# Kernel tuning notes

Hardware: AMD Instinct MI355X
Metric: run time of the kernel (lower is better)

Reference implementation:

```python
import jax, jax.numpy as jnp
import numpy as np


def setup_inputs() -> dict:
    key = jax.random.key(0)
    k1, k2 = jax.random.split(key)
    N, C, H, W = 8, 512, 64, 64
    K = 64
    x = jax.random.normal(k1, (N, C, H, W), dtype=jnp.float32)
    y = jax.random.normal(k2, (N, K, H, W), dtype=jnp.float32)
    scale = jnp.zeros((1,), dtype=jnp.float32)
    return {"x": x, "y": y, "scale": scale}


def reference(x, y, scale):
    N, C, H, W = x.shape
    K = y.shape[1]
    HW = H * W
    xq = x.reshape(N, C, HW)            # (N, C, HW) queries (channel-wise)
    yk = y.reshape(N, K, HW)            # (N, K, HW) keys/values
    # energy: (N, C, K)
    energy = jnp.einsum('ncs,nks->nck', xq, yk)
    # inverted max-subtraction: softmax(max_k(E) - E) over last dim
    energy_new = jnp.max(energy, axis=-1, keepdims=True) - energy
    attention = jax.nn.softmax(energy_new, axis=-1)  # (N, C, K)
    out = jnp.einsum('nck,nks->ncs', attention, yk)   # (N, C, HW)
    out = out.reshape(N, C, H, W)
    return x + scale * out
```

## Files before the change

### kernel.cpp

```cpp
#include <hip/hip_runtime.h>

#define N_ 8
#define C_ 512
#define K_ 64
#define HW_ 4096
#define SCHUNK 128
#define NCH 32

typedef __attribute__((ext_vector_type(8))) short short8;
typedef __attribute__((ext_vector_type(4))) float floatx4;

__device__ __forceinline__ short8 cvt8(const float* __restrict__ p){
  float4 u = *(const float4*)p;
  float4 w = *(const float4*)(p + 4);
  union { unsigned u32[4]; short8 s; } r;
  asm("v_cvt_pk_bf16_f32 %0, %1, %2" : "=v"(r.u32[0]) : "v"(u.x), "v"(u.y));
  asm("v_cvt_pk_bf16_f32 %0, %1, %2" : "=v"(r.u32[1]) : "v"(u.z), "v"(u.w));
  asm("v_cvt_pk_bf16_f32 %0, %1, %2" : "=v"(r.u32[2]) : "v"(w.x), "v"(w.y));
  asm("v_cvt_pk_bf16_f32 %0, %1, %2" : "=v"(r.u32[3]) : "v"(w.z), "v"(w.w));
  return r.s;
}

__device__ __forceinline__ void gload16(const void* g, void* l){
  __builtin_amdgcn_global_load_lds(
      (const __attribute__((address_space(1))) void*)g,
      (__attribute__((address_space(3))) void*)l, 16, 0, 0);
}

__global__ __launch_bounds__(256) void k_prep(const float* __restrict__ y,
                                              unsigned short* __restrict__ ybf,
                                              unsigned short* __restrict__ ytr){
  __shared__ unsigned short tile[64][72];
  int n  = blockIdx.x >> 6;
  int s0 = (blockIdx.x & 63) << 6;
  int tid = threadIdx.x;
  int k  = tid >> 2;
  int sc = (tid & 3) << 4;
  const float* yp = y + ((size_t)n * K_ + k) * HW_ + s0 + sc;
  union { unsigned short u16[16]; short8 s8[2]; uint4 q[2]; } u;
  u.s8[0] = cvt8(yp);
  u.s8[1] = cvt8(yp + 8);
  unsigned short* rp = ybf + ((size_t)n * K_ + k) * HW_ + s0 + sc;
  *(uint4*)rp       = u.q[0];
  *(uint4*)(rp + 8) = u.q[1];
#pragma unroll
  for (int j = 0; j < 16; ++j) tile[sc + j][k] = u.u16[j];
  __syncthreads();
  int s  = tid >> 2;
  int kc = (tid & 3) << 4;
  unsigned short* tp = ytr + ((size_t)n * HW_ + s0 + s) * K_ + kc;
  *(uint4*)tp       = *(const uint4*)&tile[s][kc];
  *(uint4*)(tp + 8) = *(const uint4*)&tile[s][kc + 8];
}

__global__ __launch_bounds__(512, 1) void k_fused(const float* __restrict__ x,
                                                  const unsigned short* __restrict__ ybf,
                                                  const unsigned short* __restrict__ ytr,
                                                  const float* __restrict__ scale,
                                                  float* __restrict__ out){
  __shared__ char As[4][8192];
  __shared__ char Bs[4][16384];
  __shared__ float Els[2][16][64];
  __shared__ char attl[2048];
  __shared__ float T[8][16][68];

  const int bid = ((blockIdx.x & 7) << 5) | (blockIdx.x >> 3);
  const int ct = bid & 31, n = bid >> 5;
  const int tid = threadIdx.x;
  const int w = tid >> 6, l = tid & 63;
  const int lo = l & 15, hi = l >> 4;
  const int h = w >> 2, q = w & 3;
  const int c0 = ct << 4;

  float sc = scale[0];
  asm volatile("" :: "v"(sc));

  const int ar = (w << 1) + (l >> 5);
  const char* asrc = (const char*)(x + ((size_t)n * C_ + c0 + ar) * HW_)
                     + ((16 * (l & 31)) ^ ((ar & 7) << 4));
  const int kb0 = ((w << 1) + 0) * 4 + (l >> 4);
  const int kb1 = ((w << 1) + 1) * 4 + (l >> 4);
  const char* bsrc0 = (const char*)(ybf + ((size_t)n * K_ + kb0) * HW_)
                      + ((16 * (l & 15)) ^ ((kb0 & 7) << 4));
  const char* bsrc1 = (const char*)(ybf + ((size_t)n * K_ + kb1) * HW_)
                      + ((16 * (l & 15)) ^ ((kb1 & 7) << 4));

  floatx4 acc = {0.f, 0.f, 0.f, 0.f};
  const int aswz = (lo & 7) << 4;
  const int brow = (q << 4) + lo;

#define STAGE(BUF, CH)                                                          \
  {                                                                             \
    gload16(asrc  + (size_t)(CH) * (SCHUNK * 4), As[BUF] + (w << 10));          \
    gload16(bsrc0 + (size_t)(CH) * (SCHUNK * 2), Bs[BUF] + ((w << 1) << 10));   \
    gload16(bsrc1 + (size_t)(CH) * (SCHUNK * 2), Bs[BUF] + ((((w << 1) | 1)) << 10)); \
  }

  STAGE(0, 0) STAGE(1, 1) STAGE(2, 2)

#pragma unroll
  for (int ch = 0; ch < NCH; ++ch){
    const int cur = ch & 3;
    if (ch + 3 < NCH){
      STAGE((ch + 3) & 3, ch + 3)
      asm volatile("s_waitcnt vmcnt(9)" ::: "memory");
    } else if (ch + 2 < NCH){
      asm volatile("s_waitcnt vmcnt(6)" ::: "memory");
    } else if (ch + 1 < NCH){
      asm volatile("s_waitcnt vmcnt(3)" ::: "memory");
    } else {
      asm volatile("s_waitcnt vmcnt(0)" ::: "memory");
    }
    __builtin_amdgcn_s_barrier();
    __builtin_amdgcn_sched_barrier(0);
#pragma unroll
    for (int ss = 0; ss < 2; ++ss){
      int ao = (h << 8) + (ss << 7) + (hi << 5);
      const char* ab = As[cur] + (lo << 9);
      float4 a0f = *(const float4*)(ab + ((ao     ) ^ aswz));
      float4 a1f = *(const float4*)(ab + ((ao + 16) ^ aswz));
      union { unsigned u32[4]; short8 s; } af;
      asm("v_cvt_pk_bf16_f32 %0, %1, %2" : "=v"(af.u32[0]) : "v"(a0f.x), "v"(a0f.y));
      asm("v_cvt_pk_bf16_f32 %0, %1, %2" : "=v"(af.u32[1]) : "v"(a0f.z), "v"(a0f.w));
      asm("v_cvt_pk_bf16_f32 %0, %1, %2" : "=v"(af.u32[2]) : "v"(a1f.x), "v"(a1f.y));
      asm("v_cvt_pk_bf16_f32 %0, %1, %2" : "=v"(af.u32[3]) : "v"(a1f.z), "v"(a1f.w));
      int bo = (h << 7) + (ss << 6) + (hi << 4);
      short8 b = *(const short8*)(Bs[cur] + brow * 256 + (bo ^ aswz));
      acc = __builtin_amdgcn_mfma_f32_16x16x32_bf16(b, af.s, acc, 0, 0, 0);
    }
    __builtin_amdgcn_sched_barrier(0);
    __builtin_amdgcn_s_barrier();
  }
#undef STAGE

  *(floatx4*)&Els[h][lo][(q << 4) + (hi << 2)] = acc;
  __syncthreads();

  if (tid < 256){
    int c = tid >> 4, j = tid & 15;
    float4 t0 = *(const float4*)&Els[0][c][4 * j];
    float4 t1 = *(const float4*)&Els[1][c][4 * j];
    float e0 = t0.x + t1.x, e1 = t0.y + t1.y, e2 = t0.z + t1.z, e3 = t0.w + t1.w;
    float m = fminf(fminf(e0, e1), fminf(e2, e3));
#pragma unroll
    for (int off = 8; off; off >>= 1) m = fminf(m, __shfl_xor(m, off, 16));
    float p0 = __expf(m - e0), p1 = __expf(m - e1);
    float p2 = __expf(m - e2), p3 = __expf(m - e3);
    float s = p0 + p1 + p2 + p3;
#pragma unroll
    for (int off = 8; off; off >>= 1) s += __shfl_xor(s, off, 16);
    float inv = 1.f / s;
    unsigned d0, d1;
    asm("v_cvt_pk_bf16_f32 %0, %1, %2" : "=v"(d0) : "v"(p0 * inv), "v"(p1 * inv));
    asm("v_cvt_pk_bf16_f32 %0, %1, %2" : "=v"(d1) : "v"(p2 * inv), "v"(p3 * inv));
    uint2 dd; dd.x = d0; dd.y = d1;
    *(uint2*)(attl + c * 128 + ((8 * j) ^ ((c & 7) << 4))) = dd;
  }
  __syncthreads();

  short8 batt0 = *(const short8*)(attl + lo * 128 + ((     hi * 16) ^ ((lo & 7) << 4)));
  short8 batt1 = *(const short8*)(attl + lo * 128 + ((64 + hi * 16) ^ ((lo & 7) << 4)));
  const unsigned short* ybn = ytr + (size_t)n * HW_ * K_;
  const int sW = w << 9;
  float (*Tw)[68] = T[w];
  size_t xb[4];
#pragma unroll
  for (int rg = 0; rg < 4; ++rg)
    xb[rg] = ((size_t)n * C_ + c0 + (rg << 2) + hi) * HW_ + sW + (lo << 2);

  short8 aA[8]; float4 xA[4];
  short8 aB[8]; float4 xB[4];

#define PVLOAD(G, AV, XV)                                                      \
  {                                                                            \
    int sg = sW + (G) * 64;                                                    \
    _Pragma("unroll")                                                          \
    for (int t = 0; t < 4; ++t){                                               \
      const unsigned short* ap = ybn + (size_t)(sg + t * 16 + lo) * K_ + (hi << 3); \
      AV[2 * t]     = *(const short8*)(ap);                                    \
      AV[2 * t + 1] = *(const short8*)(ap + 32);                               \
    }                                                                          \
    _Pragma("unroll")                                                          \
    for (int rg = 0; rg < 4; ++rg)                                             \
      XV[rg] = *(const float4*)(x + xb[rg] + (G) * 64);                        \
  }

#define PVCOMP(G, AV, XV)                                                      \
  {                                                                            \
    _Pragma("unroll")                                                          \
    for (int t = 0; t < 4; ++t){                                               \
      floatx4 a2 = {0.f, 0.f, 0.f, 0.f};                                       \
      a2 = __builtin_amdgcn_mfma_f32_16x16x32_bf16(AV[2 * t],     batt0, a2, 0, 0, 0); \
      a2 = __builtin_amdgcn_mfma_f32_16x16x32_bf16(AV[2 * t + 1], batt1, a2, 0, 0, 0); \
      *(floatx4*)&Tw[lo][t * 16 + (hi << 2)] = a2;    \
    }                                                                          \
    _Pragma("unroll")                                                          \
    for (int rg = 0; rg < 4; ++rg){                                            \
      float4 v  = *(const float4*)&Tw[(rg << 2) + hi][lo << 2];                \
      float4 xv = XV[rg];                                                      \
      float4 o;                                                                \
      o.x = xv.x + sc * v.x; o.y = xv.y + sc * v.y;                            \
      o.z = xv.z + sc * v.z; o.w = xv.w + sc * v.w;                            \
      *(float4*)(out + xb[rg] + (G) * 64) = o;                                 \
    }                                                                          \
  }

  PVLOAD(0, aA, xA)
#pragma unroll
  for (int g = 0; g < 8; g += 2){
    PVLOAD(g + 1, aB, xB)
    PVCOMP(g, aA, xA)
    if (g + 2 < 8) PVLOAD(g + 2, aA, xA)
    PVCOMP(g + 1, aB, xB)
  }
#undef PVLOAD
#undef PVCOMP
}

extern "C" void kernel_launch(void* const* d_in, const int* in_sizes, int n_in,
                              void* d_out, int out_size, void* d_ws, size_t ws_size,
                              hipStream_t stream){
  const float* x     = (const float*)d_in[0];
  const float* y     = (const float*)d_in[1];
  const float* scale = (const float*)d_in[2];
  float* out = (float*)d_out;

  char* ws = (char*)d_ws;
  unsigned short* ybf = (unsigned short*)(ws);
  unsigned short* ytr = (unsigned short*)(ws + (4u<<20));

  k_prep  <<<N_ * (HW_/64), 256, 0, stream>>>(y, ybf, ytr);
  k_fused <<<N_ * 32,       512, 0, stream>>>(x, ybf, ytr, scale, out);
}
```

Baseline: 52.00 us.

## Split spatial reduction across block pairs with global partial-energy exchange

Each (n, channel-tile) is now handled by two blocks, each reducing half of the spatial dimension. The blocks exchange partial energy sums through a global buffer, synchronising with an atomic flag and a spin wait. This doubles the grid so more of the device's compute units get work, and it cuts the LDS pipeline to two stages so more blocks fit. The cost is an inter-block dependency that relies on both partner blocks being co-resident, plus an extra memset and global traffic.

```diff
diff --git a/kernel.cpp b/kernel.cpp
--- a/kernel.cpp
+++ b/kernel.cpp
@@ -5,7 +5,7 @@
 #define K_ 64
 #define HW_ 4096
 #define SCHUNK 128
-#define NCH 32
+#define NCH 16
 
 typedef __attribute__((ext_vector_type(8))) short short8;
 typedef __attribute__((ext_vector_type(4))) float floatx4;
@@ -53,60 +53,58 @@
   *(uint4*)(tp + 8) = *(const uint4*)&tile[s][kc + 8];
 }
 
-__global__ __launch_bounds__(512, 1) void k_fused(const float* __restrict__ x,
+__global__ __launch_bounds__(512, 4) void k_fused(const float* __restrict__ x,
                                                   const unsigned short* __restrict__ ybf,
                                                   const unsigned short* __restrict__ ytr,
                                                   const float* __restrict__ scale,
+                                                  unsigned* __restrict__ flags,
+                                                  float* __restrict__ epart,
                                                   float* __restrict__ out){
-  __shared__ char As[4][8192];
-  __shared__ char Bs[4][16384];
-  __shared__ float Els[2][16][64];
-  __shared__ char attl[2048];
-  __shared__ float T[8][16][68];
-
-  const int bid = ((blockIdx.x & 7) << 5) | (blockIdx.x >> 3);
-  const int ct = bid & 31, n = bid >> 5;
+  __shared__ char smem[49152];
+
+  const int b = blockIdx.x;
+  const int n = b >> 6, ct = (b >> 1) & 31, half = b & 1;
   const int tid = threadIdx.x;
   const int w = tid >> 6, l = tid & 63;
   const int lo = l & 15, hi = l >> 4;
   const int h = w >> 2, q = w & 3;
   const int c0 = ct << 4;
+  const int sb = half << 11;
+  const int pairid = (n << 5) + ct;
 
   float sc = scale[0];
   asm volatile("" :: "v"(sc));
 
   const int ar = (w << 1) + (l >> 5);
-  const char* asrc = (const char*)(x + ((size_t)n * C_ + c0 + ar) * HW_)
+  const char* asrc = (const char*)(x + ((size_t)n * C_ + c0 + ar) * HW_ + sb)
                      + ((16 * (l & 31)) ^ ((ar & 7) << 4));
   const int kb0 = ((w << 1) + 0) * 4 + (l >> 4);
   const int kb1 = ((w << 1) + 1) * 4 + (l >> 4);
-  const char* bsrc0 = (const char*)(ybf + ((size_t)n * K_ + kb0) * HW_)
+  const char* bsrc0 = (const char*)(ybf + ((size_t)n * K_ + kb0) * HW_ + sb)
                       + ((16 * (l & 15)) ^ ((kb0 & 7) << 4));
-  const char* bsrc1 = (const char*)(ybf + ((size_t)n * K_ + kb1) * HW_)
+  const char* bsrc1 = (const char*)(ybf + ((size_t)n * K_ + kb1) * HW_ + sb)
                       + ((16 * (l & 15)) ^ ((kb1 & 7) << 4));
 
   floatx4 acc = {0.f, 0.f, 0.f, 0.f};
   const int aswz = (lo & 7) << 4;
   const int brow = (q << 4) + lo;
 
-#define STAGE(BUF, CH)                                                          \
-  {                                                                             \
-    gload16(asrc  + (size_t)(CH) * (SCHUNK * 4), As[BUF] + (w << 10));          \
-    gload16(bsrc0 + (size_t)(CH) * (SCHUNK * 2), Bs[BUF] + ((w << 1) << 10));   \
-    gload16(bsrc1 + (size_t)(CH) * (SCHUNK * 2), Bs[BUF] + ((((w << 1) | 1)) << 10)); \
-  }
-
-  STAGE(0, 0) STAGE(1, 1) STAGE(2, 2)
+#define AS(BUF) (smem + (BUF) * 24576)
+#define BS(BUF) (smem + (BUF) * 24576 + 8192)
+#define STAGE(BUF, CH)                                                         \
+  {                                                                            \
+    gload16(asrc  + (size_t)(CH) * (SCHUNK * 4), AS(BUF) + (w << 10));         \
+    gload16(bsrc0 + (size_t)(CH) * (SCHUNK * 2), BS(BUF) + ((w << 1) << 10));  \
+    gload16(bsrc1 + (size_t)(CH) * (SCHUNK * 2), BS(BUF) + (((w << 1) | 1) << 10)); \
+  }
+
+  STAGE(0, 0)
 
 #pragma unroll
   for (int ch = 0; ch < NCH; ++ch){
-    const int cur = ch & 3;
-    if (ch + 3 < NCH){
-      STAGE((ch + 3) & 3, ch + 3)
-      asm volatile("s_waitcnt vmcnt(9)" ::: "memory");
-    } else if (ch + 2 < NCH){
-      asm volatile("s_waitcnt vmcnt(6)" ::: "memory");
-    } else if (ch + 1 < NCH){
+    const int cur = ch & 1;
+    if (ch + 1 < NCH){
+      STAGE(cur ^ 1, ch + 1)
       asm volatile("s_waitcnt vmcnt(3)" ::: "memory");
     } else {
       asm volatile("s_waitcnt vmcnt(0)" ::: "memory");
@@ -116,7 +114,7 @@
 #pragma unroll
     for (int ss = 0; ss < 2; ++ss){
       int ao = (h << 8) + (ss << 7) + (hi << 5);
-      const char* ab = As[cur] + (lo << 9);
+      const char* ab = AS(cur) + (lo << 9);
       float4 a0f = *(const float4*)(ab + ((ao     ) ^ aswz));
       float4 a1f = *(const float4*)(ab + ((ao + 16) ^ aswz));
       union { unsigned u32[4]; short8 s; } af;
@@ -125,22 +123,47 @@
       asm("v_cvt_pk_bf16_f32 %0, %1, %2" : "=v"(af.u32[2]) : "v"(a1f.x), "v"(a1f.y));
       asm("v_cvt_pk_bf16_f32 %0, %1, %2" : "=v"(af.u32[3]) : "v"(a1f.z), "v"(a1f.w));
       int bo = (h << 7) + (ss << 6) + (hi << 4);
-      short8 b = *(const short8*)(Bs[cur] + brow * 256 + (bo ^ aswz));
-      acc = __builtin_amdgcn_mfma_f32_16x16x32_bf16(b, af.s, acc, 0, 0, 0);
+      short8 bfr = *(const short8*)(BS(cur) + brow * 256 + (bo ^ aswz));
+      acc = __builtin_amdgcn_mfma_f32_16x16x32_bf16(bfr, af.s, acc, 0, 0, 0);
     }
     __builtin_amdgcn_sched_barrier(0);
     __builtin_amdgcn_s_barrier();
   }
 #undef STAGE
 
+  float (*Els)[16][64] = (float (*)[16][64])smem;
   *(floatx4*)&Els[h][lo][(q << 4) + (hi << 2)] = acc;
   __syncthreads();
 
+  float e0 = 0.f, e1 = 0.f, e2 = 0.f, e3 = 0.f;
   if (tid < 256){
+    float4 t0 = *(const float4*)&Els[0][tid >> 4][(tid & 15) * 4];
+    float4 t1 = *(const float4*)&Els[1][tid >> 4][(tid & 15) * 4];
+    e0 = t0.x + t1.x; e1 = t0.y + t1.y; e2 = t0.z + t1.z; e3 = t0.w + t1.w;
+    float* ep = epart + (((size_t)pairid << 1) + half) * 1024 + (tid << 2);
+    __hip_atomic_store(ep + 0, e0, __ATOMIC_RELAXED, __HIP_MEMORY_SCOPE_AGENT);
+    __hip_atomic_store(ep + 1, e1, __ATOMIC_RELAXED, __HIP_MEMORY_SCOPE_AGENT);
+    __hip_atomic_store(ep + 2, e2, __ATOMIC_RELAXED, __HIP_MEMORY_SCOPE_AGENT);
+    __hip_atomic_store(ep + 3, e3, __ATOMIC_RELAXED, __HIP_MEMORY_SCOPE_AGENT);
+  }
+  __threadfence();
+  __syncthreads();
+  if (tid == 0){
+    atomicAdd(&flags[pairid], 1u);
+    while (atomicAdd(&flags[pairid], 0u) < 2u)
+      __builtin_amdgcn_s_sleep(1);
+  }
+  __syncthreads();
+  __threadfence();
+
+  char* attl = smem + 8192;
+  if (tid < 256){
+    const float* ep = epart + (((size_t)pairid << 1) + (half ^ 1)) * 1024 + (tid << 2);
+    e0 += __hip_atomic_load(ep + 0, __ATOMIC_RELAXED, __HIP_MEMORY_SCOPE_AGENT);
+    e1 += __hip_atomic_load(ep + 1, __ATOMIC_RELAXED, __HIP_MEMORY_SCOPE_AGENT);
+    e2 += __hip_atomic_load(ep + 2, __ATOMIC_RELAXED, __HIP_MEMORY_SCOPE_AGENT);
+    e3 += __hip_atomic_load(ep + 3, __ATOMIC_RELAXED, __HIP_MEMORY_SCOPE_AGENT);
     int c = tid >> 4, j = tid & 15;
-    float4 t0 = *(const float4*)&Els[0][c][4 * j];
-    float4 t1 = *(const float4*)&Els[1][c][4 * j];
-    float e0 = t0.x + t1.x, e1 = t0.y + t1.y, e2 = t0.z + t1.z, e3 = t0.w + t1.w;
     float m = fminf(fminf(e0, e1), fminf(e2, e3));
 #pragma unroll
     for (int off = 8; off; off >>= 1) m = fminf(m, __shfl_xor(m, off, 16));
@@ -161,19 +184,19 @@
   short8 batt0 = *(const short8*)(attl + lo * 128 + ((     hi * 16) ^ ((lo & 7) << 4)));
   short8 batt1 = *(const short8*)(attl + lo * 128 + ((64 + hi * 16) ^ ((lo & 7) << 4)));
   const unsigned short* ybn = ytr + (size_t)n * HW_ * K_;
-  const int sW = w << 9;
-  float (*Tw)[68] = T[w];
+  const int sP = sb + (w << 8);
+  float (*Tw)[68] = (float (*)[68])(smem + 16384 + w * 4352);
   size_t xb[4];
 #pragma unroll
   for (int rg = 0; rg < 4; ++rg)
-    xb[rg] = ((size_t)n * C_ + c0 + (rg << 2) + hi) * HW_ + sW + (lo << 2);
+    xb[rg] = ((size_t)n * C_ + c0 + (rg << 2) + hi) * HW_ + sP + (lo << 2);
 
   short8 aA[8]; float4 xA[4];
   short8 aB[8]; float4 xB[4];
 
 #define PVLOAD(G, AV, XV)                                                      \
   {                                                                            \
-    int sg = sW + (G) * 64;                                                    \
+    int sg = sP + (G) * 64;                                                    \
     _Pragma("unroll")                                                          \
     for (int t = 0; t < 4; ++t){                                               \
       const unsigned short* ap = ybn + (size_t)(sg + t * 16 + lo) * K_ + (hi << 3); \
@@ -206,15 +229,17 @@
   }
 
   PVLOAD(0, aA, xA)
-#pragma unroll
-  for (int g = 0; g < 8; g += 2){
-    PVLOAD(g + 1, aB, xB)
-    PVCOMP(g, aA, xA)
-    if (g + 2 < 8) PVLOAD(g + 2, aA, xA)
-    PVCOMP(g + 1, aB, xB)
-  }
+  PVLOAD(1, aB, xB)
+  PVCOMP(0, aA, xA)
+  PVLOAD(2, aA, xA)
+  PVCOMP(1, aB, xB)
+  PVLOAD(3, aB, xB)
+  PVCOMP(2, aA, xA)
+  PVCOMP(3, aB, xB)
 #undef PVLOAD
 #undef PVCOMP
+#undef AS
+#undef BS
 }
 
 extern "C" void kernel_launch(void* const* d_in, const int* in_sizes, int n_in,
@@ -226,9 +251,12 @@
   float* out = (float*)d_out;
 
   char* ws = (char*)d_ws;
-  unsigned short* ybf = (unsigned short*)(ws);
-  unsigned short* ytr = (unsigned short*)(ws + (4u<<20));
-
+  unsigned*       flags = (unsigned*)(ws);
+  float*          epart = (float*)(ws + 4096);
+  unsigned short* ybf   = (unsigned short*)(ws + (4u<<20));
+  unsigned short* ytr   = (unsigned short*)(ws + (8u<<20));
+
+  hipMemsetAsync(flags, 0, 1024, stream);
   k_prep  <<<N_ * (HW_/64), 256, 0, stream>>>(y, ybf, ytr);
-  k_fused <<<N_ * 32,       512, 0, stream>>>(x, ybf, ytr, scale, out);
-}
+  k_fused <<<N_ * 32 * 2,   512, 0, stream>>>(x, ybf, ytr, scale, flags, epart, out);
+}
```

Result: slower. 187.4 us (+260.4%).

## Split channel tiles in half to double grid and cut LDS for occupancy

Applied to the files above, without the earlier changes.

Each block now handles 8 channels instead of 16, which doubles the grid to 512 blocks. The staging pipeline drops from four buffers to two, and LDS is shared in one union buffer so several blocks can fit per CU (launch bounds raised to 4). The 16-wide MFMA tiles are kept, so the extra rows are padded with zeros or masked on store, which wastes half the MFMA work and re-reads y for each half. The aim is more parallelism and latency hiding on a GPU whose 256 blocks left many CUs underused, at the cost of a shallower prefetch pipeline and duplicated y traffic.

```diff
diff --git a/kernel.cpp b/kernel.cpp
--- a/kernel.cpp
+++ b/kernel.cpp
@@ -53,30 +53,28 @@
   *(uint4*)(tp + 8) = *(const uint4*)&tile[s][kc + 8];
 }
 
-__global__ __launch_bounds__(512, 1) void k_fused(const float* __restrict__ x,
+__global__ __launch_bounds__(512, 4) void k_fused(const float* __restrict__ x,
                                                   const unsigned short* __restrict__ ybf,
                                                   const unsigned short* __restrict__ ytr,
                                                   const float* __restrict__ scale,
                                                   float* __restrict__ out){
-  __shared__ char As[4][8192];
-  __shared__ char Bs[4][16384];
-  __shared__ float Els[2][16][64];
+  __shared__ char stg[40960];
+  __shared__ float Els[2][8][64];
   __shared__ char attl[2048];
-  __shared__ float T[8][16][68];
-
-  const int bid = ((blockIdx.x & 7) << 5) | (blockIdx.x >> 3);
-  const int ct = bid & 31, n = bid >> 5;
+
+  const int bid = ((blockIdx.x & 7) << 6) | (blockIdx.x >> 3);
+  const int chf = bid & 1, ct = (bid >> 1) & 31, n = bid >> 6;
   const int tid = threadIdx.x;
   const int w = tid >> 6, l = tid & 63;
   const int lo = l & 15, hi = l >> 4;
   const int h = w >> 2, q = w & 3;
-  const int c0 = ct << 4;
+  const int c0 = (ct << 4) + (chf << 3);
 
   float sc = scale[0];
   asm volatile("" :: "v"(sc));
 
   const int ar = (w << 1) + (l >> 5);
-  const char* asrc = (const char*)(x + ((size_t)n * C_ + c0 + ar) * HW_)
+  const char* asrc = (const char*)(x + ((size_t)n * C_ + c0 + (ar & 7)) * HW_)
                      + ((16 * (l & 31)) ^ ((ar & 7) << 4));
   const int kb0 = ((w << 1) + 0) * 4 + (l >> 4);
   const int kb1 = ((w << 1) + 1) * 4 + (l >> 4);
@@ -89,25 +87,25 @@
   const int aswz = (lo & 7) << 4;
   const int brow = (q << 4) + lo;
 
-#define STAGE(BUF, CH)                                                          \
-  {                                                                             \
-    gload16(asrc  + (size_t)(CH) * (SCHUNK * 4), As[BUF] + (w << 10));          \
-    gload16(bsrc0 + (size_t)(CH) * (SCHUNK * 2), Bs[BUF] + ((w << 1) << 10));   \
-    gload16(bsrc1 + (size_t)(CH) * (SCHUNK * 2), Bs[BUF] + ((((w << 1) | 1)) << 10)); \
-  }
-
-  STAGE(0, 0) STAGE(1, 1) STAGE(2, 2)
+#define AS(BUF) (stg + (BUF) * 20480)
+#define BS(BUF) (stg + (BUF) * 20480 + 4096)
+#define STAGE(BUF, CH)                                                         \
+  {                                                                            \
+    if (w < 4)                                                                 \
+      gload16(asrc  + (size_t)(CH) * (SCHUNK * 4), AS(BUF) + (w << 10));       \
+    gload16(bsrc0 + (size_t)(CH) * (SCHUNK * 2), BS(BUF) + ((w << 1) << 10));  \
+    gload16(bsrc1 + (size_t)(CH) * (SCHUNK * 2), BS(BUF) + (((w << 1) | 1) << 10)); \
+  }
+
+  STAGE(0, 0)
 
 #pragma unroll
   for (int ch = 0; ch < NCH; ++ch){
-    const int cur = ch & 3;
-    if (ch + 3 < NCH){
-      STAGE((ch + 3) & 3, ch + 3)
-      asm volatile("s_waitcnt vmcnt(9)" ::: "memory");
-    } else if (ch + 2 < NCH){
-      asm volatile("s_waitcnt vmcnt(6)" ::: "memory");
-    } else if (ch + 1 < NCH){
-      asm volatile("s_waitcnt vmcnt(3)" ::: "memory");
+    const int cur = ch & 1;
+    if (ch + 1 < NCH){
+      STAGE(cur ^ 1, ch + 1)
+      if (w < 4) asm volatile("s_waitcnt vmcnt(3)" ::: "memory");
+      else       asm volatile("s_waitcnt vmcnt(2)" ::: "memory");
     } else {
       asm volatile("s_waitcnt vmcnt(0)" ::: "memory");
     }
@@ -116,7 +114,7 @@
 #pragma unroll
     for (int ss = 0; ss < 2; ++ss){
       int ao = (h << 8) + (ss << 7) + (hi << 5);
-      const char* ab = As[cur] + (lo << 9);
+      const char* ab = AS(cur) + (lo << 9);
       float4 a0f = *(const float4*)(ab + ((ao     ) ^ aswz));
       float4 a1f = *(const float4*)(ab + ((ao + 16) ^ aswz));
       union { unsigned u32[4]; short8 s; } af;
@@ -125,18 +123,19 @@
       asm("v_cvt_pk_bf16_f32 %0, %1, %2" : "=v"(af.u32[2]) : "v"(a1f.x), "v"(a1f.y));
       asm("v_cvt_pk_bf16_f32 %0, %1, %2" : "=v"(af.u32[3]) : "v"(a1f.z), "v"(a1f.w));
       int bo = (h << 7) + (ss << 6) + (hi << 4);
-      short8 b = *(const short8*)(Bs[cur] + brow * 256 + (bo ^ aswz));
-      acc = __builtin_amdgcn_mfma_f32_16x16x32_bf16(b, af.s, acc, 0, 0, 0);
+      short8 bfr = *(const short8*)(BS(cur) + brow * 256 + (bo ^ aswz));
+      acc = __builtin_amdgcn_mfma_f32_16x16x32_bf16(bfr, af.s, acc, 0, 0, 0);
     }
     __builtin_amdgcn_sched_barrier(0);
     __builtin_amdgcn_s_barrier();
   }
 #undef STAGE
 
-  *(floatx4*)&Els[h][lo][(q << 4) + (hi << 2)] = acc;
+  if (lo < 8)
+    *(floatx4*)&Els[h][lo][(q << 4) + (hi << 2)] = acc;
   __syncthreads();
 
-  if (tid < 256){
+  if (tid < 128){
     int c = tid >> 4, j = tid & 15;
     float4 t0 = *(const float4*)&Els[0][c][4 * j];
     float4 t1 = *(const float4*)&Els[1][c][4 * j];
@@ -155,25 +154,29 @@
     asm("v_cvt_pk_bf16_f32 %0, %1, %2" : "=v"(d1) : "v"(p2 * inv), "v"(p3 * inv));
     uint2 dd; dd.x = d0; dd.y = d1;
     *(uint2*)(attl + c * 128 + ((8 * j) ^ ((c & 7) << 4))) = dd;
+  } else if (tid < 256){
+    int c = tid >> 4, j = tid & 15;
+    uint2 z; z.x = 0u; z.y = 0u;
+    *(uint2*)(attl + c * 128 + ((8 * j) ^ ((c & 7) << 4))) = z;
   }
   __syncthreads();
 
   short8 batt0 = *(const short8*)(attl + lo * 128 + ((     hi * 16) ^ ((lo & 7) << 4)));
   short8 batt1 = *(const short8*)(attl + lo * 128 + ((64 + hi * 16) ^ ((lo & 7) << 4)));
   const unsigned short* ybn = ytr + (size_t)n * HW_ * K_;
-  const int sW = w << 9;
-  float (*Tw)[68] = T[w];
-  size_t xb[4];
-#pragma unroll
-  for (int rg = 0; rg < 4; ++rg)
-    xb[rg] = ((size_t)n * C_ + c0 + (rg << 2) + hi) * HW_ + sW + (lo << 2);
-
-  short8 aA[8]; float4 xA[4];
-  short8 aB[8]; float4 xB[4];
+  const int sP = w << 9;
+  float (*Tw)[68] = (float (*)[68])(stg + w * 2176);
+  size_t xb[2];
+#pragma unroll
+  for (int rg = 0; rg < 2; ++rg)
+    xb[rg] = ((size_t)n * C_ + c0 + (rg << 2) + hi) * HW_ + sP + (lo << 2);
+
+  short8 aA[8]; float4 xA[2];
+  short8 aB[8]; float4 xB[2];
 
 #define PVLOAD(G, AV, XV)                                                      \
   {                                                                            \
-    int sg = sW + (G) * 64;                                                    \
+    int sg = sP + (G) * 64;                                                    \
     _Pragma("unroll")                                                          \
     for (int t = 0; t < 4; ++t){                                               \
       const unsigned short* ap = ybn + (size_t)(sg + t * 16 + lo) * K_ + (hi << 3); \
@@ -181,7 +184,7 @@
       AV[2 * t + 1] = *(const short8*)(ap + 32);                               \
     }                                                                          \
     _Pragma("unroll")                                                          \
-    for (int rg = 0; rg < 4; ++rg)                                             \
+    for (int rg = 0; rg < 2; ++rg)                                             \
       XV[rg] = *(const float4*)(x + xb[rg] + (G) * 64);                        \
   }
 
@@ -192,10 +195,11 @@
       floatx4 a2 = {0.f, 0.f, 0.f, 0.f};                                       \
       a2 = __builtin_amdgcn_mfma_f32_16x16x32_bf16(AV[2 * t],     batt0, a2, 0, 0, 0); \
       a2 = __builtin_amdgcn_mfma_f32_16x16x32_bf16(AV[2 * t + 1], batt1, a2, 0, 0, 0); \
-      *(floatx4*)&Tw[lo][t * 16 + (hi << 2)] = a2;    \
+      if (lo < 8)                                                              \
+        *(floatx4*)&Tw[lo][t * 16 + (hi << 2)] = a2;   \
     }                                                                          \
     _Pragma("unroll")                                                          \
-    for (int rg = 0; rg < 4; ++rg){                                            \
+    for (int rg = 0; rg < 2; ++rg){                                            \
       float4 v  = *(const float4*)&Tw[(rg << 2) + hi][lo << 2];                \
       float4 xv = XV[rg];                                                      \
       float4 o;                                                                \
@@ -215,6 +219,8 @@
   }
 #undef PVLOAD
 #undef PVCOMP
+#undef AS
+#undef BS
 }
 
 extern "C" void kernel_launch(void* const* d_in, const int* in_sizes, int n_in,
@@ -230,5 +236,5 @@
   unsigned short* ytr = (unsigned short*)(ws + (4u<<20));
 
   k_prep  <<<N_ * (HW_/64), 256, 0, stream>>>(y, ybf, ytr);
-  k_fused <<<N_ * 32,       512, 0, stream>>>(x, ybf, ytr, scale, out);
-}
+  k_fused <<<N_ * 32 * 2,   512, 0, stream>>>(x, ybf, ytr, scale, out);
+}
```

Result: slower. 63.49 us (+22.1%).
